# Performance work log

Measured on AMD Instinct MI355X. Metric: run time of the kernel, lower is better.

The kernel has to match this reference:

```python
import jax, jax.numpy as jnp
import numpy as np

HEADS = 16
DIM_HEAD = 64


def setup_inputs() -> dict:
    key = jax.random.key(0)
    k1, k2, k3 = jax.random.split(key, 3)
    b, n, dim = 4, 2048, 1024
    inner = HEADS * DIM_HEAD  # 1024
    x = jax.random.normal(k1, (b, n, dim), dtype=jnp.float32)
    # Dense weights, scaled like Glorot-ish init to keep softmax well-behaved
    w_qkv = jax.random.normal(k2, (dim, 3 * inner), dtype=jnp.float32) * (dim ** -0.5)
    w_out = jax.random.normal(k3, (inner, dim), dtype=jnp.float32) * (inner ** -0.5)
    b_out = jnp.zeros((dim,), dtype=jnp.float32)
    return {"x": x, "w_qkv": w_qkv, "w_out": w_out, "b_out": b_out}


def reference(x, w_qkv, w_out, b_out):
    b, n, dim = x.shape
    scale = DIM_HEAD ** -0.5
    qkv = x @ w_qkv  # [b, n, 3*h*d]
    q, k, v = jnp.split(qkv, 3, axis=-1)
    # 'b n (h d) -> b h n d'
    split_heads = lambda t: t.reshape(b, n, HEADS, DIM_HEAD).transpose(0, 2, 1, 3)
    q, k, v = split_heads(q), split_heads(k), split_heads(v)
    sim = jnp.einsum('bhid,bhjd->bhij', q, k) * scale  # [b, h, n, n]
    attn = jax.nn.softmax(sim, axis=-1)
    out = jnp.einsum('bhij,bhjd->bhid', attn, v)  # [b, h, n, d]
    out = out.transpose(0, 2, 1, 3).reshape(b, n, HEADS * DIM_HEAD)
    return out @ w_out + b_out  # dropout rate 0.0 -> identity
```

## Files before the change

### kernel.cpp

```cpp
#include <hip/hip_runtime.h>
#include <cstdint>

#define HEADS 16
#define DH 64
#define SEQ 2048
#define BATCH 4
#define DIM 1024
#define MTOT (BATCH*SEQ)
#define NQKV (3*DIM)

typedef short bf16x8 __attribute__((ext_vector_type(8)));
typedef float f32x4 __attribute__((ext_vector_type(4)));
typedef float f32x16 __attribute__((ext_vector_type(16)));

__device__ __forceinline__ unsigned short f2bf(float f) {
  union { float fv; unsigned int u; } c; c.fv = f;
  unsigned int u = c.u;
  u += 0x7FFFu + ((u >> 16) & 1u);
  return (unsigned short)(u >> 16);
}

__device__ __forceinline__ unsigned int pkbf(float lo, float hi) {
  union { float fv; unsigned int u; } a, b; a.fv = lo; b.fv = hi;
  return ((a.u + 0x8000u) >> 16) | ((b.u + 0x8000u) & 0xFFFF0000u);
}

__device__ __forceinline__ f32x4 mfma16(bf16x8 a, bf16x8 b, f32x4 c) {
  return __builtin_amdgcn_mfma_f32_16x16x32_bf16(a, b, c, 0, 0, 0);
}
__device__ __forceinline__ f32x16 mfma32(bf16x8 a, bf16x8 b, f32x16 c) {
  return __builtin_amdgcn_mfma_f32_32x32x16_bf16(a, b, c, 0, 0, 0);
}

typedef const __attribute__((address_space(1))) unsigned int* gas_ptr;
typedef __attribute__((address_space(3))) unsigned int* las_ptr;
__device__ __forceinline__ void gl2lds16(const void* g, void* l) {
  __builtin_amdgcn_global_load_lds((gas_ptr)g, (las_ptr)l, 16, 0, 0);
}

#define QSCALE 0.18033688011112042f

__global__ __launch_bounds__(256) void cast_f32_bf16(
    const float* __restrict__ in, unsigned short* __restrict__ out, int n4) {
  int i = blockIdx.x * blockDim.x + threadIdx.x;
  if (i >= n4) return;
  float4 v = reinterpret_cast<const float4*>(in)[i];
  uint2 o;
  o.x = (unsigned int)f2bf(v.x) | ((unsigned int)f2bf(v.y) << 16);
  o.y = (unsigned int)f2bf(v.z) | ((unsigned int)f2bf(v.w) << 16);
  reinterpret_cast<uint2*>(out)[i] = o;
}

__global__ __launch_bounds__(256) void transpose_cast(
    const float* __restrict__ in, unsigned short* __restrict__ out, int R, int C) {
  __shared__ float tile[32][33];
  int c0 = blockIdx.x * 32, r0 = blockIdx.y * 32;
  int tx = threadIdx.x & 31, ty = threadIdx.x >> 5;
  for (int i = 0; i < 32; i += 8)
    tile[ty + i][tx] = in[(size_t)(r0 + ty + i) * C + c0 + tx];
  __syncthreads();
  for (int i = 0; i < 32; i += 8)
    out[(size_t)(c0 + ty + i) * R + r0 + tx] = f2bf(tile[tx][ty + i]);
}

__global__ __launch_bounds__(256) void transpose_v(
    const unsigned short* __restrict__ V, unsigned short* __restrict__ Vt) {
  __shared__ unsigned short tile[64][72];
  int n0 = blockIdx.x * 64;
  size_t base = (size_t)blockIdx.y * SEQ * DH;
  int t = threadIdx.x;
  int r = t >> 2, c = (t & 3) * 8;
  *(uint4*)&tile[r][c]      = *(const uint4*)&V[base + (size_t)(n0 + r) * DH + c];
  *(uint4*)&tile[r][c + 32] = *(const uint4*)&V[base + (size_t)(n0 + r) * DH + c + 32];
  __syncthreads();
#pragma unroll
  for (int p = 0; p < 2; p++) {
    alignas(16) unsigned short tmp[8];
#pragma unroll
    for (int i = 0; i < 8; i++) tmp[i] = tile[c + p * 32 + i][r];
    *(uint4*)&Vt[base + (size_t)r * SEQ + n0 + c + p * 32] = *(uint4*)tmp;
  }
}

#define BM 128
#define BN 128
#define BK 32
#define LDT 32

__global__ __launch_bounds__(256) void gemm_qkv(
    const unsigned short* __restrict__ A, const unsigned short* __restrict__ Bt,
    unsigned short* __restrict__ Q, unsigned short* __restrict__ K,
    unsigned short* __restrict__ V) {
  __shared__ unsigned short sA[BM * LDT];
  __shared__ unsigned short sB[BN * LDT];
  const int KD = 1024;
  int m0 = blockIdx.y * BM;
  int n0 = blockIdx.x * BN;
  int t = threadIdx.x;
  int lane = t & 63, w = t >> 6;
  int wm = (w >> 1) * 64, wn = (w & 1) * 64;
  int fr = lane & 15, fq = (lane >> 4) * 8;

  const unsigned short* gA = &A[(size_t)(m0 + w * 16 + (lane >> 2)) * KD + (lane & 3) * 8];
  const unsigned short* gB = &Bt[(size_t)(n0 + w * 16 + (lane >> 2)) * KD + (lane & 3) * 8];
  char* lA = (char*)sA + w * 1024;
  char* lB = (char*)sB + w * 1024;

  f32x4 acc[4][4];
#pragma unroll
  for (int i = 0; i < 4; i++)
#pragma unroll
    for (int j = 0; j < 4; j++) { f32x4 z = {0.f, 0.f, 0.f, 0.f}; acc[i][j] = z; }

  for (int k0 = 0; k0 < KD; k0 += BK) {
    gl2lds16(gA + k0, lA);
    gl2lds16(gA + (size_t)64 * KD + k0, lA + 4096);
    gl2lds16(gB + k0, lB);
    gl2lds16(gB + (size_t)64 * KD + k0, lB + 4096);
    __syncthreads();
    bf16x8 af[4], bfr[4];
#pragma unroll
    for (int mt = 0; mt < 4; mt++)
      af[mt] = *reinterpret_cast<const bf16x8*>(&sA[(wm + mt * 16 + fr) * LDT + fq]);
#pragma unroll
    for (int nt = 0; nt < 4; nt++)
      bfr[nt] = *reinterpret_cast<const bf16x8*>(&sB[(wn + nt * 16 + fr) * LDT + fq]);
#pragma unroll
    for (int mt = 0; mt < 4; mt++)
#pragma unroll
      for (int nt = 0; nt < 4; nt++)
        acc[mt][nt] = mfma16(af[mt], bfr[nt], acc[mt][nt]);
    __syncthreads();
  }
  int rowq = (lane >> 4) * 4;
#pragma unroll
  for (int mt = 0; mt < 4; mt++)
#pragma unroll
    for (int nt = 0; nt < 4; nt++)
#pragma unroll
      for (int r = 0; r < 4; r++) {
        int m = m0 + wm + mt * 16 + rowq + r;
        int ncol = n0 + wn + nt * 16 + fr;
        int which = ncol >> 10;
        int hd = ncol & 1023;
        int b = m >> 11, nrow = m & 2047;
        float v = acc[mt][nt][r];
        if (which == 0) v *= QSCALE;
        unsigned short* dst = (which == 0) ? Q : (which == 1 ? K : V);
        size_t idx = ((size_t)(b * HEADS + (hd >> 6)) * SEQ + nrow) * DH + (hd & 63);
        dst[idx] = f2bf(v);
      }
}

__global__ __launch_bounds__(256) void gemm_out(
    const unsigned short* __restrict__ A, const unsigned short* __restrict__ Bt,
    const float* __restrict__ bias, float* __restrict__ C) {
  __shared__ unsigned short sA[BM * LDT];
  __shared__ unsigned short sB[BN * LDT];
  const int KD = 1024;
  int m0 = blockIdx.y * BM;
  int n0 = blockIdx.x * BN;
  int t = threadIdx.x;
  int lane = t & 63, w = t >> 6;
  int wm = (w >> 1) * 64, wn = (w & 1) * 64;
  int fr = lane & 15, fq = (lane >> 4) * 8;

  const unsigned short* gA = &A[(size_t)(m0 + w * 16 + (lane >> 2)) * KD + (lane & 3) * 8];
  const unsigned short* gB = &Bt[(size_t)(n0 + w * 16 + (lane >> 2)) * KD + (lane & 3) * 8];
  char* lA = (char*)sA + w * 1024;
  char* lB = (char*)sB + w * 1024;

  f32x4 acc[4][4];
#pragma unroll
  for (int i = 0; i < 4; i++)
#pragma unroll
    for (int j = 0; j < 4; j++) { f32x4 z = {0.f, 0.f, 0.f, 0.f}; acc[i][j] = z; }

  for (int k0 = 0; k0 < KD; k0 += BK) {
    gl2lds16(gA + k0, lA);
    gl2lds16(gA + (size_t)64 * KD + k0, lA + 4096);
    gl2lds16(gB + k0, lB);
    gl2lds16(gB + (size_t)64 * KD + k0, lB + 4096);
    __syncthreads();
    bf16x8 af[4], bfr[4];
#pragma unroll
    for (int mt = 0; mt < 4; mt++)
      af[mt] = *reinterpret_cast<const bf16x8*>(&sA[(wm + mt * 16 + fr) * LDT + fq]);
#pragma unroll
    for (int nt = 0; nt < 4; nt++)
      bfr[nt] = *reinterpret_cast<const bf16x8*>(&sB[(wn + nt * 16 + fr) * LDT + fq]);
#pragma unroll
    for (int mt = 0; mt < 4; mt++)
#pragma unroll
      for (int nt = 0; nt < 4; nt++)
        acc[mt][nt] = mfma16(af[mt], bfr[nt], acc[mt][nt]);
    __syncthreads();
  }
  int rowq = (lane >> 4) * 4;
#pragma unroll
  for (int mt = 0; mt < 4; mt++)
#pragma unroll
    for (int nt = 0; nt < 4; nt++)
#pragma unroll
      for (int r = 0; r < 4; r++) {
        int m = m0 + wm + mt * 16 + rowq + r;
        int ncol = n0 + wn + nt * 16 + fr;
        C[(size_t)m * DIM + ncol] = acc[mt][nt][r] + bias[ncol];
      }
}

#define LDA 72

__global__ __launch_bounds__(256, 4) void attention(
    const unsigned short* __restrict__ Qg, const unsigned short* __restrict__ Kg,
    const unsigned short* __restrict__ Vtg, unsigned short* __restrict__ Og) {
  __shared__ unsigned short sK[64 * LDA];
  __shared__ unsigned short sVt[64 * LDA];
  __shared__ unsigned short sP[4 * 32 * LDA];
  int qb = blockIdx.x, h = blockIdx.y, b = blockIdx.z;
  size_t base = (size_t)(b * HEADS + h) * SEQ * DH;
  const unsigned short* Q = Qg + base;
  const unsigned short* K = Kg + base;
  const unsigned short* Vt = Vtg + base;
  int t = threadIdx.x, lane = t & 63, w = t >> 6;
  int m = lane & 31, kh = lane >> 5;
  int q0 = qb * 128 + w * 32;

  bf16x8 qf[4];
#pragma unroll
  for (int kt = 0; kt < 4; kt++)
    qf[kt] = *reinterpret_cast<const bf16x8*>(&Q[(size_t)(q0 + m) * DH + kt * 16 + kh * 8]);

  bf16x8 ones;
#pragma unroll
  for (int i = 0; i < 8; i++) ones[i] = (short)0x3F80;

  f32x16 oacc0, oacc1, rsacc;
#pragma unroll
  for (int i = 0; i < 16; i++) { oacc0[i] = 0.f; oacc1[i] = 0.f; rsacc[i] = 0.f; }

  unsigned short* sPw = &sP[w * 32 * LDA];
  int sr = t >> 2, sc = (t & 3) * 8;

  for (int j0 = 0; j0 < SEQ; j0 += 64) {
    *(uint4*)&sK[sr * LDA + sc]       = *(const uint4*)&K[(size_t)(j0 + sr) * DH + sc];
    *(uint4*)&sK[sr * LDA + sc + 32]  = *(const uint4*)&K[(size_t)(j0 + sr) * DH + sc + 32];
    *(uint4*)&sVt[sr * LDA + sc]      = *(const uint4*)&Vt[(size_t)sr * SEQ + j0 + sc];
    *(uint4*)&sVt[sr * LDA + sc + 32] = *(const uint4*)&Vt[(size_t)sr * SEQ + j0 + sc + 32];
    __syncthreads();

#pragma unroll
    for (int jt = 0; jt < 2; jt++) {
      f32x16 s;
#pragma unroll
      for (int i = 0; i < 16; i++) s[i] = 0.f;
#pragma unroll
      for (int kt = 0; kt < 4; kt++) {
        bf16x8 kf = *reinterpret_cast<const bf16x8*>(&sK[(jt * 32 + m) * LDA + kt * 16 + kh * 8]);
        s = mfma32(kf, qf[kt], s);
      }
#pragma unroll
      for (int p = 0; p < 4; p++) {
        float e0 = __builtin_amdgcn_exp2f(s[4 * p + 0]);
        float e1 = __builtin_amdgcn_exp2f(s[4 * p + 1]);
        float e2 = __builtin_amdgcn_exp2f(s[4 * p + 2]);
        float e3 = __builtin_amdgcn_exp2f(s[4 * p + 3]);
        uint2 pk; pk.x = pkbf(e0, e1); pk.y = pkbf(e2, e3);
        *(uint2*)&sPw[m * LDA + jt * 32 + 8 * p + 4 * kh] = pk;
      }
    }

#pragma unroll
    for (int jc = 0; jc < 4; jc++) {
      bf16x8 pf = *reinterpret_cast<const bf16x8*>(&sPw[m * LDA + jc * 16 + kh * 8]);
      bf16x8 v0 = *reinterpret_cast<const bf16x8*>(&sVt[m * LDA + jc * 16 + kh * 8]);
      bf16x8 v1 = *reinterpret_cast<const bf16x8*>(&sVt[(32 + m) * LDA + jc * 16 + kh * 8]);
      rsacc = mfma32(pf, ones, rsacc);
      oacc0 = mfma32(pf, v0, oacc0);
      oacc1 = mfma32(pf, v1, oacc1);
    }
    __syncthreads();
  }

#pragma unroll
  for (int reg = 0; reg < 16; reg++) {
    int row = (reg & 3) + 8 * (reg >> 2) + 4 * kh;
    float inv = 1.0f / rsacc[reg];
    int n = q0 + row;
    size_t o = ((size_t)(b * SEQ + n)) * DIM + h * DH;
    Og[o + m]      = f2bf(oacc0[reg] * inv);
    Og[o + 32 + m] = f2bf(oacc1[reg] * inv);
  }
}

extern "C" void kernel_launch(void* const* d_in, const int* in_sizes, int n_in,
                              void* d_out, int out_size, void* d_ws, size_t ws_size,
                              hipStream_t stream) {
  const float* x     = (const float*)d_in[0];
  const float* w_qkv = (const float*)d_in[1];
  const float* w_out = (const float*)d_in[2];
  const float* b_out = (const float*)d_in[3];
  float* out = (float*)d_out;

  char* ws = (char*)d_ws;
  unsigned short* xb     = (unsigned short*)ws; ws += (size_t)MTOT * DIM * 2;
  unsigned short* wqkv_t = (unsigned short*)ws; ws += (size_t)NQKV * DIM * 2;
  unsigned short* wout_t = (unsigned short*)ws; ws += (size_t)DIM * DIM * 2;
  unsigned short* qb_    = (unsigned short*)ws; ws += (size_t)BATCH * HEADS * SEQ * DH * 2;
  unsigned short* kb_    = (unsigned short*)ws; ws += (size_t)BATCH * HEADS * SEQ * DH * 2;
  unsigned short* vb_    = (unsigned short*)ws; ws += (size_t)BATCH * HEADS * SEQ * DH * 2;
  unsigned short* attnb  = (unsigned short*)ws; ws += (size_t)MTOT * DIM * 2;
  unsigned short* vt_    = xb;

  cast_f32_bf16<<<(MTOT * DIM / 4 + 255) / 256, 256, 0, stream>>>(x, xb, MTOT * DIM / 4);
  transpose_cast<<<dim3(NQKV / 32, DIM / 32), 256, 0, stream>>>(w_qkv, wqkv_t, DIM, NQKV);
  transpose_cast<<<dim3(DIM / 32, DIM / 32), 256, 0, stream>>>(w_out, wout_t, DIM, DIM);

  gemm_qkv<<<dim3(NQKV / BN, MTOT / BM), 256, 0, stream>>>(xb, wqkv_t, qb_, kb_, vb_);

  transpose_v<<<dim3(SEQ / 64, BATCH * HEADS), 256, 0, stream>>>(vb_, vt_);

  attention<<<dim3(SEQ / 128, HEADS, BATCH), 256, 0, stream>>>(qb_, kb_, vt_, attnb);

  gemm_out<<<dim3(DIM / BN, MTOT / BM), 256, 0, stream>>>(attnb, wout_t, b_out, out);
}
```

Measured before the change: 305.1 us.

## Process two query tiles per wave in attention and swizzle LDS layouts

Each wave now handles 64 query rows instead of 32, so every K and V fragment read from LDS feeds two sets of MFMAs. This halves K/V global and LDS traffic per query. An XOR swizzle is applied to the sK, sVt and sP LDS layouts to reduce bank conflicts. The cost is more registers (launch bounds drop to 2 blocks per SM), a larger sP buffer, and half as many blocks in the grid, which lowers occupancy.

```diff
diff --git a/kernel.cpp b/kernel.cpp
--- a/kernel.cpp
+++ b/kernel.cpp
@@ -210,13 +210,14 @@
 }
 
 #define LDA 72
-
-__global__ __launch_bounds__(256, 4) void attention(
+#define SW(r, c) ((c) ^ (((r) >> 3) & 3))
+
+__global__ __launch_bounds__(256, 2) void attention(
     const unsigned short* __restrict__ Qg, const unsigned short* __restrict__ Kg,
     const unsigned short* __restrict__ Vtg, unsigned short* __restrict__ Og) {
   __shared__ unsigned short sK[64 * LDA];
   __shared__ unsigned short sVt[64 * LDA];
-  __shared__ unsigned short sP[4 * 32 * LDA];
+  __shared__ unsigned short sP[4 * 64 * LDA];
   int qb = blockIdx.x, h = blockIdx.y, b = blockIdx.z;
   size_t base = (size_t)(b * HEADS + h) * SEQ * DH;
   const unsigned short* Q = Qg + base;
@@ -224,73 +225,93 @@
   const unsigned short* Vt = Vtg + base;
   int t = threadIdx.x, lane = t & 63, w = t >> 6;
   int m = lane & 31, kh = lane >> 5;
-  int q0 = qb * 128 + w * 32;
-
-  bf16x8 qf[4];
-#pragma unroll
-  for (int kt = 0; kt < 4; kt++)
-    qf[kt] = *reinterpret_cast<const bf16x8*>(&Q[(size_t)(q0 + m) * DH + kt * 16 + kh * 8]);
+  int q0 = qb * 256 + w * 64;
+  int ksw = (m >> 3) & 3;
+
+  bf16x8 qf[2][4];
+#pragma unroll
+  for (int qh = 0; qh < 2; qh++)
+#pragma unroll
+    for (int kt = 0; kt < 4; kt++)
+      qf[qh][kt] = *reinterpret_cast<const bf16x8*>(
+          &Q[(size_t)(q0 + 32 * qh + m) * DH + kt * 16 + kh * 8]);
 
   bf16x8 ones;
 #pragma unroll
   for (int i = 0; i < 8; i++) ones[i] = (short)0x3F80;
 
-  f32x16 oacc0, oacc1, rsacc;
-#pragma unroll
-  for (int i = 0; i < 16; i++) { oacc0[i] = 0.f; oacc1[i] = 0.f; rsacc[i] = 0.f; }
-
-  unsigned short* sPw = &sP[w * 32 * LDA];
-  int sr = t >> 2, sc = (t & 3) * 8;
+  f32x16 oacc[2][2], rsacc[2];
+#pragma unroll
+  for (int qh = 0; qh < 2; qh++) {
+#pragma unroll
+    for (int i = 0; i < 16; i++) { oacc[qh][0][i] = 0.f; oacc[qh][1][i] = 0.f; rsacc[qh][i] = 0.f; }
+  }
+
+  unsigned short* sPw = &sP[w * 64 * LDA];
+  int sr = t >> 2, sc = t & 3;
 
   for (int j0 = 0; j0 < SEQ; j0 += 64) {
-    *(uint4*)&sK[sr * LDA + sc]       = *(const uint4*)&K[(size_t)(j0 + sr) * DH + sc];
-    *(uint4*)&sK[sr * LDA + sc + 32]  = *(const uint4*)&K[(size_t)(j0 + sr) * DH + sc + 32];
-    *(uint4*)&sVt[sr * LDA + sc]      = *(const uint4*)&Vt[(size_t)sr * SEQ + j0 + sc];
-    *(uint4*)&sVt[sr * LDA + sc + 32] = *(const uint4*)&Vt[(size_t)sr * SEQ + j0 + sc + 32];
+    *(uint4*)&sK[sr * LDA + SW(sr, sc) * 8]      = *(const uint4*)&K[(size_t)(j0 + sr) * DH + sc * 8];
+    *(uint4*)&sK[sr * LDA + SW(sr, sc + 4) * 8]  = *(const uint4*)&K[(size_t)(j0 + sr) * DH + (sc + 4) * 8];
+    *(uint4*)&sVt[sr * LDA + SW(sr, sc) * 8]     = *(const uint4*)&Vt[(size_t)sr * SEQ + j0 + sc * 8];
+    *(uint4*)&sVt[sr * LDA + SW(sr, sc + 4) * 8] = *(const uint4*)&Vt[(size_t)sr * SEQ + j0 + (sc + 4) * 8];
     __syncthreads();
 
 #pragma unroll
     for (int jt = 0; jt < 2; jt++) {
-      f32x16 s;
-#pragma unroll
-      for (int i = 0; i < 16; i++) s[i] = 0.f;
-#pragma unroll
-      for (int kt = 0; kt < 4; kt++) {
-        bf16x8 kf = *reinterpret_cast<const bf16x8*>(&sK[(jt * 32 + m) * LDA + kt * 16 + kh * 8]);
-        s = mfma32(kf, qf[kt], s);
-      }
-#pragma unroll
-      for (int p = 0; p < 4; p++) {
-        float e0 = __builtin_amdgcn_exp2f(s[4 * p + 0]);
-        float e1 = __builtin_amdgcn_exp2f(s[4 * p + 1]);
-        float e2 = __builtin_amdgcn_exp2f(s[4 * p + 2]);
-        float e3 = __builtin_amdgcn_exp2f(s[4 * p + 3]);
-        uint2 pk; pk.x = pkbf(e0, e1); pk.y = pkbf(e2, e3);
-        *(uint2*)&sPw[m * LDA + jt * 32 + 8 * p + 4 * kh] = pk;
+      bf16x8 kf[4];
+#pragma unroll
+      for (int kt = 0; kt < 4; kt++)
+        kf[kt] = *reinterpret_cast<const bf16x8*>(
+            &sK[(jt * 32 + m) * LDA + SW(m, 2 * kt + kh) * 8]);
+#pragma unroll
+      for (int qh = 0; qh < 2; qh++) {
+        f32x16 s;
+#pragma unroll
+        for (int i = 0; i < 16; i++) s[i] = 0.f;
+#pragma unroll
+        for (int kt = 0; kt < 4; kt++)
+          s = mfma32(kf[kt], qf[qh][kt], s);
+        int prow = 32 * qh + m;
+#pragma unroll
+        for (int p = 0; p < 4; p++) {
+          float e0 = __builtin_amdgcn_exp2f(s[4 * p + 0]);
+          float e1 = __builtin_amdgcn_exp2f(s[4 * p + 1]);
+          float e2 = __builtin_amdgcn_exp2f(s[4 * p + 2]);
+          float e3 = __builtin_amdgcn_exp2f(s[4 * p + 3]);
+          uint2 pk; pk.x = pkbf(e0, e1); pk.y = pkbf(e2, e3);
+          *(uint2*)&sPw[prow * LDA + ((4 * jt + p) ^ ksw) * 8 + 4 * kh] = pk;
+        }
       }
     }
 
 #pragma unroll
     for (int jc = 0; jc < 4; jc++) {
-      bf16x8 pf = *reinterpret_cast<const bf16x8*>(&sPw[m * LDA + jc * 16 + kh * 8]);
-      bf16x8 v0 = *reinterpret_cast<const bf16x8*>(&sVt[m * LDA + jc * 16 + kh * 8]);
-      bf16x8 v1 = *reinterpret_cast<const bf16x8*>(&sVt[(32 + m) * LDA + jc * 16 + kh * 8]);
-      rsacc = mfma32(pf, ones, rsacc);
-      oacc0 = mfma32(pf, v0, oacc0);
-      oacc1 = mfma32(pf, v1, oacc1);
+      bf16x8 v0 = *reinterpret_cast<const bf16x8*>(&sVt[m * LDA + ((2 * jc + kh) ^ ksw) * 8]);
+      bf16x8 v1 = *reinterpret_cast<const bf16x8*>(&sVt[(32 + m) * LDA + ((2 * jc + kh) ^ ksw) * 8]);
+#pragma unroll
+      for (int qh = 0; qh < 2; qh++) {
+        int prow = 32 * qh + m;
+        bf16x8 pf = *reinterpret_cast<const bf16x8*>(&sPw[prow * LDA + ((2 * jc + kh) ^ ksw) * 8]);
+        rsacc[qh]    = mfma32(pf, ones, rsacc[qh]);
+        oacc[qh][0]  = mfma32(pf, v0, oacc[qh][0]);
+        oacc[qh][1]  = mfma32(pf, v1, oacc[qh][1]);
+      }
     }
     __syncthreads();
   }
 
 #pragma unroll
-  for (int reg = 0; reg < 16; reg++) {
-    int row = (reg & 3) + 8 * (reg >> 2) + 4 * kh;
-    float inv = 1.0f / rsacc[reg];
-    int n = q0 + row;
-    size_t o = ((size_t)(b * SEQ + n)) * DIM + h * DH;
-    Og[o + m]      = f2bf(oacc0[reg] * inv);
-    Og[o + 32 + m] = f2bf(oacc1[reg] * inv);
-  }
+  for (int qh = 0; qh < 2; qh++)
+#pragma unroll
+    for (int reg = 0; reg < 16; reg++) {
+      int row = (reg & 3) + 8 * (reg >> 2) + 4 * kh;
+      float inv = 1.0f / rsacc[qh][reg];
+      int n = q0 + 32 * qh + row;
+      size_t o = ((size_t)(b * SEQ + n)) * DIM + h * DH;
+      Og[o + m]      = f2bf(oacc[qh][0][reg] * inv);
+      Og[o + 32 + m] = f2bf(oacc[qh][1][reg] * inv);
+    }
 }
 
 extern "C" void kernel_launch(void* const* d_in, const int* in_sizes, int n_in,
@@ -320,7 +341,7 @@
 
   transpose_v<<<dim3(SEQ / 64, BATCH * HEADS), 256, 0, stream>>>(vb_, vt_);
 
-  attention<<<dim3(SEQ / 128, HEADS, BATCH), 256, 0, stream>>>(qb_, kb_, vt_, attnb);
+  attention<<<dim3(SEQ / 256, HEADS, BATCH), 256, 0, stream>>>(qb_, kb_, vt_, attnb);
 
   gemm_out<<<dim3(DIM / BN, MTOT / BM), 256, 0, stream>>>(attnb, wout_t, b_out, out);
 }
```

After: 290.2 us. 1.05x faster.
